# Optimization experiments

Measured on AMD Instinct MI355X. Metric: run time of the kernel, lower is better.

The kernel has to match this reference:

```python
import jax, jax.numpy as jnp
import numpy as np

V = 50000

def _spmm(edge_vals, edge_row, edge_col, x):
    # sparse (V,V) @ dense (V,F) via gather + segment_sum
    return jax.ops.segment_sum(edge_vals[:, None] * x[edge_col], edge_row, num_segments=V)

def setup_inputs() -> dict:
    key = jax.random.key(0)
    ks = jax.random.split(key, 6)
    B, Cin, Cout, K, E = 4, 128, 128, 4, 800000
    x = jax.random.normal(ks[0], (B, Cin, V), dtype=jnp.float32)
    edge_row = jax.random.randint(ks[1], (E,), 0, V, dtype=jnp.int32)
    edge_col = jax.random.randint(ks[2], (E,), 0, V, dtype=jnp.int32)
    edge_vals = jax.random.normal(ks[3], (E,), dtype=jnp.float32) * 0.05
    std = np.sqrt(2.0 / (Cin * K)).astype(np.float32)
    weights = jax.random.normal(ks[4], (K, Cin, Cout), dtype=jnp.float32) * std
    biases = jnp.full((Cout,), 0.01, dtype=jnp.float32)
    return {"x": x, "edge_row": edge_row, "edge_col": edge_col,
            "edge_vals": edge_vals, "weights": weights, "biases": biases}

def reference(x, edge_row, edge_col, edge_vals, weights, biases):
    B, Cin, Vv = x.shape
    K = weights.shape[0]
    # (B,Cin,V) -> (V, B*Cin)
    x0 = jnp.transpose(x, (2, 0, 1)).reshape(Vv, B * Cin)
    xs = [x0]
    if K > 1:
        x1 = _spmm(edge_vals, edge_row, edge_col, x0)
        xs.append(x1)
        for _ in range(2, K):
            x2 = 2.0 * _spmm(edge_vals, edge_row, edge_col, x1) - x0
            xs.append(x2)
            x0, x1 = x1, x2
    xk = jnp.stack(xs, 0).reshape(K, Vv, B, Cin)
    # tensordot over (K, Cin): (K,V,B,Cin) x (K,Cin,Cout) -> (V,B,Cout)
    out = jnp.einsum('kvbc,kco->vbo', xk, weights)
    out = out + biases
    # permute (V,B,Cout) -> (B,Cout,V)
    return jnp.transpose(out, (1, 2, 0))
```

## Files before the change

kernel.cpp:

```cpp
#include <hip/hip_runtime.h>

#define V_N   50000
#define B_N   4
#define C_IN  128
#define C_OUT 128
#define E_N   800000
#define F_N   512
#define M_TOT 200000

#define SCAN_BLK  1024
#define SCAN_NB   ((V_N + SCAN_BLK - 1) / SCAN_BLK)

typedef unsigned short ushort_t;
typedef __attribute__((ext_vector_type(8))) short short8;
typedef __attribute__((ext_vector_type(4))) float f32x4;

__device__ __forceinline__ float bf_lo(unsigned u) { return __uint_as_float(u << 16); }
__device__ __forceinline__ float bf_hi(unsigned u) { return __uint_as_float(u & 0xFFFF0000u); }
__device__ __forceinline__ ushort_t f2bf(float f) {
    unsigned u = __float_as_uint(f);
    u += 0x7FFFu + ((u >> 16) & 1u);
    return (ushort_t)(u >> 16);
}

__global__ __launch_bounds__(256) void k_transpose_in(const float* __restrict__ x,
                                                      ushort_t* __restrict__ x0) {
    __shared__ float tile[32][33];
    int vb = blockIdx.x * 32;
    int fb = blockIdx.y * 32;
    int tx = threadIdx.x, ty = threadIdx.y;
#pragma unroll
    for (int i = 0; i < 32; i += 8) {
        int f = fb + ty + i, v = vb + tx;
        float val = 0.f;
        if (v < V_N) val = x[(size_t)f * V_N + v];
        tile[ty + i][tx] = val;
    }
    __syncthreads();
#pragma unroll
    for (int i = 0; i < 32; i += 8) {
        int v = vb + ty + i, f = fb + tx;
        if (v < V_N) x0[(size_t)v * F_N + f] = f2bf(tile[tx][ty + i]);
    }
}

__global__ __launch_bounds__(256) void k_hist(const int* __restrict__ row,
                                              int* __restrict__ counts) {
    int e = blockIdx.x * blockDim.x + threadIdx.x;
    if (e < E_N) atomicAdd(&counts[row[e]], 1);
}

__global__ __launch_bounds__(256) void k_scan_blk(const int* __restrict__ counts,
                                                  int* __restrict__ row_ptr,
                                                  int* __restrict__ blk_sums) {
    __shared__ int s[256];
    int t = threadIdx.x;
    int base = blockIdx.x * SCAN_BLK + t * 4;
    int c0 = (base + 0 < V_N) ? counts[base + 0] : 0;
    int c1 = (base + 1 < V_N) ? counts[base + 1] : 0;
    int c2 = (base + 2 < V_N) ? counts[base + 2] : 0;
    int c3 = (base + 3 < V_N) ? counts[base + 3] : 0;
    int p1 = c0, p2 = c0 + c1, p3 = c0 + c1 + c2, tot = p3 + c3;
    s[t] = tot;
    __syncthreads();
#pragma unroll
    for (int off = 1; off < 256; off <<= 1) {
        int v = (t >= off) ? s[t - off] : 0;
        __syncthreads();
        s[t] += v;
        __syncthreads();
    }
    int excl = (t == 0) ? 0 : s[t - 1];
    if (base + 0 < V_N) row_ptr[base + 0] = excl;
    if (base + 1 < V_N) row_ptr[base + 1] = excl + p1;
    if (base + 2 < V_N) row_ptr[base + 2] = excl + p2;
    if (base + 3 < V_N) row_ptr[base + 3] = excl + p3;
    if (t == 255) blk_sums[blockIdx.x] = s[255];
}

__global__ __launch_bounds__(64) void k_scan_top(const int* __restrict__ blk_sums,
                                                 int* __restrict__ blk_off) {
    int t = threadIdx.x;
    int v = (t < SCAN_NB) ? blk_sums[t] : 0;
#pragma unroll
    for (int off = 1; off < 64; off <<= 1) {
        int u = __shfl_up(v, off);
        if (t >= off) v += u;
    }
    blk_off[t] = v;
}

__global__ __launch_bounds__(256) void k_scan_add(const int* __restrict__ blk_off,
                                                  int* __restrict__ row_ptr,
                                                  int* __restrict__ next) {
    int b = blockIdx.x, t = threadIdx.x;
    int off = (b == 0) ? 0 : blk_off[b - 1];
    int base = b * SCAN_BLK + t * 4;
#pragma unroll
    for (int i = 0; i < 4; i++) {
        int idx = base + i;
        if (idx < V_N) {
            int rv = row_ptr[idx] + off;
            row_ptr[idx] = rv;
            next[idx]    = rv;
        }
    }
    if (b == 0 && t == 0) row_ptr[V_N] = blk_off[SCAN_NB - 1];
}

__global__ __launch_bounds__(256) void k_scatter(const int* __restrict__ row,
                                                 const int* __restrict__ col,
                                                 const float* __restrict__ vals,
                                                 int* __restrict__ next,
                                                 int2* __restrict__ edges) {
    int e = blockIdx.x * blockDim.x + threadIdx.x;
    if (e < E_N) {
        int r = row[e];
        int pos = atomicAdd(&next[r], 1);
        edges[pos] = make_int2(col[e], __float_as_int(vals[e]));
    }
}

__global__ __launch_bounds__(256) void k_wprep(const float* __restrict__ W,
                                               ushort_t* __restrict__ Wt) {
    int i = blockIdx.x * 256 + threadIdx.x;
    int k = i >> 14, c = (i >> 7) & 127, o = i & 127;
    Wt[((size_t)k * 128 + o) * 128 + c] = f2bf(W[i]);
}

__global__ __launch_bounds__(256) void k_spmm_bf16(const int* __restrict__ row_ptr,
                                                   const int2* __restrict__ edges,
                                                   const ushort_t* __restrict__ src,
                                                   const ushort_t* __restrict__ prev,
                                                   ushort_t* __restrict__ dst,
                                                   float alpha, float beta,
                                                   int has_prev) {
    int lane = threadIdx.x & 63;
    int g = blockIdx.x * 4 + (threadIdx.x >> 6);
    int r = g >> 1;
    int h = g & 1;
    int e0 = row_ptr[r], e1 = row_ptr[r + 1];
    float a0 = 0.f, a1 = 0.f, a2 = 0.f, a3 = 0.f;
    const ushort_t* sp = src + h * 256 + lane * 4;

    int e = e0;
    for (; e + 4 <= e1; e += 4) {
        int2 E0 = edges[e], E1 = edges[e + 1], E2 = edges[e + 2], E3 = edges[e + 3];
        uint2 g0 = *(const uint2*)(sp + (size_t)E0.x * F_N);
        uint2 g1 = *(const uint2*)(sp + (size_t)E1.x * F_N);
        uint2 g2 = *(const uint2*)(sp + (size_t)E2.x * F_N);
        uint2 g3 = *(const uint2*)(sp + (size_t)E3.x * F_N);
        float w0 = __int_as_float(E0.y), w1 = __int_as_float(E1.y);
        float w2 = __int_as_float(E2.y), w3 = __int_as_float(E3.y);
        a0 += w0 * bf_lo(g0.x); a1 += w0 * bf_hi(g0.x);
        a2 += w0 * bf_lo(g0.y); a3 += w0 * bf_hi(g0.y);
        a0 += w1 * bf_lo(g1.x); a1 += w1 * bf_hi(g1.x);
        a2 += w1 * bf_lo(g1.y); a3 += w1 * bf_hi(g1.y);
        a0 += w2 * bf_lo(g2.x); a1 += w2 * bf_hi(g2.x);
        a2 += w2 * bf_lo(g2.y); a3 += w2 * bf_hi(g2.y);
        a0 += w3 * bf_lo(g3.x); a1 += w3 * bf_hi(g3.x);
        a2 += w3 * bf_lo(g3.y); a3 += w3 * bf_hi(g3.y);
    }
    for (; e < e1; e++) {
        int2 E = edges[e];
        uint2 gv = *(const uint2*)(sp + (size_t)E.x * F_N);
        float w = __int_as_float(E.y);
        a0 += w * bf_lo(gv.x); a1 += w * bf_hi(gv.x);
        a2 += w * bf_lo(gv.y); a3 += w * bf_hi(gv.y);
    }

    size_t off = (size_t)r * F_N + h * 256 + lane * 4;
    if (has_prev) {
        uint2 pv = *(const uint2*)(prev + off);
        a0 = alpha * a0 + beta * bf_lo(pv.x);
        a1 = alpha * a1 + beta * bf_hi(pv.x);
        a2 = alpha * a2 + beta * bf_lo(pv.y);
        a3 = alpha * a3 + beta * bf_hi(pv.y);
    } else {
        a0 *= alpha; a1 *= alpha; a2 *= alpha; a3 *= alpha;
    }
    ushort_t res[4] = {f2bf(a0), f2bf(a1), f2bf(a2), f2bf(a3)};
    *(uint2*)(dst + off) = *(const uint2*)res;
}

__global__ __launch_bounds__(256, 2) void k_gemm_mfma(
        const ushort_t* __restrict__ X0, const ushort_t* __restrict__ X1,
        const ushort_t* __restrict__ X2, const ushort_t* __restrict__ X3,
        const ushort_t* __restrict__ Wt, const float* __restrict__ bias,
        float* __restrict__ out) {
    __shared__ ushort_t As[128][40];
    __shared__ ushort_t Bs[128][40];
    __shared__ float    Cs[64][133];

    int tid  = threadIdx.x;
    int lane = tid & 63;
    int wave = tid >> 6;
    int wm = wave >> 1, wn = wave & 1;
    int quad = lane >> 4, l15 = lane & 15;
    int m_blk = blockIdx.x * 128;

    f32x4 acc[4][4];
#pragma unroll
    for (int fi = 0; fi < 4; fi++)
#pragma unroll
        for (int fj = 0; fj < 4; fj++) {
            acc[fi][fj][0] = 0.f; acc[fi][fj][1] = 0.f;
            acc[fi][fj][2] = 0.f; acc[fi][fj][3] = 0.f;
        }

    const ushort_t* Xb[4] = {X0, X1, X2, X3};

    for (int kb = 0; kb < 4; kb++) {
        const ushort_t* A = Xb[kb];
        const ushort_t* W = Wt + (size_t)kb * (128 * 128);
        for (int kk = 0; kk < 128; kk += 32) {
            __syncthreads();
#pragma unroll
            for (int i = 0; i < 2; i++) {
                int id = tid + i * 256;
                int rr = id >> 2, p = id & 3;
                int gm = m_blk + rr; if (gm >= M_TOT) gm = M_TOT - 1;
                *(uint4*)&As[rr][p * 8] = *(const uint4*)&A[(size_t)gm * 128 + kk + p * 8];
                *(uint4*)&Bs[rr][p * 8] = *(const uint4*)&W[(size_t)rr * 128 + kk + p * 8];
            }
            __syncthreads();
            short8 a[4], b[4];
#pragma unroll
            for (int f = 0; f < 4; f++) {
                a[f] = *(const short8*)&As[wm * 64 + f * 16 + l15][quad * 8];
                b[f] = *(const short8*)&Bs[wn * 64 + f * 16 + l15][quad * 8];
            }
#pragma unroll
            for (int fi = 0; fi < 4; fi++)
#pragma unroll
                for (int fj = 0; fj < 4; fj++)
                    acc[fi][fj] = __builtin_amdgcn_mfma_f32_16x16x32_bf16(
                        a[fi], b[fj], acc[fi][fj], 0, 0, 0);
        }
    }

    int v_blk = m_blk >> 2;
    for (int h = 0; h < 2; h++) {
        __syncthreads();
        if (wm == h) {
#pragma unroll
            for (int fi = 0; fi < 4; fi++)
#pragma unroll
                for (int fj = 0; fj < 4; fj++) {
                    int ml = fi * 16 + quad * 4;
                    int n  = wn * 64 + fj * 16 + l15;
#pragma unroll
                    for (int reg = 0; reg < 4; reg++)
                        Cs[ml + reg][n] = acc[fi][fj][reg];
                }
        }
        __syncthreads();
#pragma unroll
        for (int i = 0; i < 8; i++) {
            int idx = tid + i * 256;
            int v4  = idx & 3;
            int o   = (idx >> 2) & 127;
            int b   = idx >> 9;
            int vl  = v4 * 4;
            float bv = bias[o];
            float r0 = Cs[(vl + 0) * 4 + b][o] + bv;
            float r1 = Cs[(vl + 1) * 4 + b][o] + bv;
            float r2 = Cs[(vl + 2) * 4 + b][o] + bv;
            float r3 = Cs[(vl + 3) * 4 + b][o] + bv;
            int v0 = v_blk + h * 16 + vl;
            float* op = out + ((size_t)b * C_OUT + o) * V_N + v0;
            if (v0 + 3 < V_N) {
                *(float4*)op = make_float4(r0, r1, r2, r3);
            } else {
                if (v0     < V_N) op[0] = r0;
                if (v0 + 1 < V_N) op[1] = r1;
                if (v0 + 2 < V_N) op[2] = r2;
                if (v0 + 3 < V_N) op[3] = r3;
            }
        }
    }
}

extern "C" void kernel_launch(void* const* d_in, const int* in_sizes, int n_in,
                              void* d_out, int out_size, void* d_ws, size_t ws_size,
                              hipStream_t stream) {
    const float* x        = (const float*)d_in[0];
    const int*   edge_row = (const int*)  d_in[1];
    const int*   edge_col = (const int*)  d_in[2];
    const float* edge_val = (const float*)d_in[3];
    const float* weights  = (const float*)d_in[4];
    const float* biases   = (const float*)d_in[5];
    float* out = (float*)d_out;

    const size_t XSZ = (size_t)V_N * F_N;
    ushort_t* x0 = (ushort_t*)d_ws;
    ushort_t* x1 = x0 + XSZ;
    ushort_t* x2 = x1 + XSZ;
    ushort_t* x3 = x2 + XSZ;
    ushort_t* Wt = x3 + XSZ;
    int* iw      = (int*)(Wt + 4 * 128 * 128);
    int* row_ptr = iw;
    int* counts  = iw + 50016;
    int* nxt     = iw + 100032;
    int* blk_sums= iw + 150048;
    int* blk_off = iw + 150112;
    int2* edges  = (int2*)(iw + 150176);

    dim3 tb(32, 8);
    dim3 tgrid((V_N + 31) / 32, F_N / 32);

    k_transpose_in<<<tgrid, tb, 0, stream>>>(x, x0);

    hipMemsetAsync(counts, 0, V_N * sizeof(int), stream);
    k_hist<<<(E_N + 255) / 256, 256, 0, stream>>>(edge_row, counts);
    k_scan_blk<<<SCAN_NB, 256, 0, stream>>>(counts, row_ptr, blk_sums);
    k_scan_top<<<1, 64, 0, stream>>>(blk_sums, blk_off);
    k_scan_add<<<SCAN_NB, 256, 0, stream>>>(blk_off, row_ptr, nxt);
    k_scatter<<<(E_N + 255) / 256, 256, 0, stream>>>(edge_row, edge_col, edge_val,
                                                     nxt, edges);

    k_wprep<<<256, 256, 0, stream>>>(weights, Wt);

    k_spmm_bf16<<<V_N * 2 / 4, 256, 0, stream>>>(row_ptr, edges, x0, x0, x1,
                                                 1.f, 0.f, 0);
    k_spmm_bf16<<<V_N * 2 / 4, 256, 0, stream>>>(row_ptr, edges, x1, x0, x2,
                                                 2.f, -1.f, 1);
    k_spmm_bf16<<<V_N * 2 / 4, 256, 0, stream>>>(row_ptr, edges, x2, x1, x3,
                                                 2.f, -1.f, 1);

    k_gemm_mfma<<<(M_TOT + 127) / 128, 256, 0, stream>>>(x0, x1, x2, x3, Wt,
                                                         biases, out);
}
```

Before: 724.6 us.

## Use direct global-to-LDS loads with XOR swizzle and K=64 tiles in GEMM

The MFMA GEMM now loads A and W tiles straight into shared memory with global_load_lds (16-byte) instead of staging them through registers. K-steps are widened from 32 to 64, which halves the number of barrier pairs. An XOR swizzle on 16-byte column groups replaces the padded layout to avoid LDS bank conflicts. This adds LDS footprint (64-wide rows) and relies on the per-wave contiguous LDS write pattern of the direct-load instruction, but the GEMM is likely a minor part of a runtime dominated by the SpMM stages.

```diff
diff --git a/kernel.cpp b/kernel.cpp
--- a/kernel.cpp
+++ b/kernel.cpp
@@ -14,6 +14,13 @@
 typedef unsigned short ushort_t;
 typedef __attribute__((ext_vector_type(8))) short short8;
 typedef __attribute__((ext_vector_type(4))) float f32x4;
+
+#define AS1 __attribute__((address_space(1)))
+#define AS3 __attribute__((address_space(3)))
+__device__ __forceinline__ void gl_lds16(const void* gp, void* lp) {
+    __builtin_amdgcn_global_load_lds((const AS1 unsigned int*)gp,
+                                     (AS3 unsigned int*)lp, 16, 0, 0);
+}
 
 __device__ __forceinline__ float bf_lo(unsigned u) { return __uint_as_float(u << 16); }
 __device__ __forceinline__ float bf_hi(unsigned u) { return __uint_as_float(u & 0xFFFF0000u); }
@@ -188,14 +195,14 @@
         const ushort_t* __restrict__ X2, const ushort_t* __restrict__ X3,
         const ushort_t* __restrict__ Wt, const float* __restrict__ bias,
         float* __restrict__ out) {
-    __shared__ ushort_t As[128][40];
-    __shared__ ushort_t Bs[128][40];
+    __shared__ ushort_t As[128][64];
+    __shared__ ushort_t Bs[128][64];
     __shared__ float    Cs[64][133];
 
     int tid  = threadIdx.x;
     int lane = tid & 63;
-    int wave = tid >> 6;
-    int wm = wave >> 1, wn = wave & 1;
+    int wv   = tid >> 6;
+    int wm = wv >> 1, wn = wv & 1;
     int quad = lane >> 4, l15 = lane & 15;
     int m_blk = blockIdx.x * 128;
 
@@ -210,32 +217,44 @@
 
     const ushort_t* Xb[4] = {X0, X1, X2, X3};
 
+    int rr_s = lane >> 3;
+    int pl   = lane & 7;
     for (int kb = 0; kb < 4; kb++) {
         const ushort_t* A = Xb[kb];
         const ushort_t* W = Wt + (size_t)kb * (128 * 128);
-        for (int kk = 0; kk < 128; kk += 32) {
+        for (int kk = 0; kk < 128; kk += 64) {
             __syncthreads();
 #pragma unroll
-            for (int i = 0; i < 2; i++) {
-                int id = tid + i * 256;
-                int rr = id >> 2, p = id & 3;
+            for (int i = 0; i < 4; i++) {
+                int r0 = (wv * 4 + i) * 8;
+                int rr = r0 + rr_s;
+                int pg = pl ^ (rr & 7);
                 int gm = m_blk + rr; if (gm >= M_TOT) gm = M_TOT - 1;
-                *(uint4*)&As[rr][p * 8] = *(const uint4*)&A[(size_t)gm * 128 + kk + p * 8];
-                *(uint4*)&Bs[rr][p * 8] = *(const uint4*)&W[(size_t)rr * 128 + kk + p * 8];
+                gl_lds16(&A[(size_t)gm * 128 + kk + pg * 8], &As[r0][0]);
+                gl_lds16(&W[(size_t)rr * 128 + kk + pg * 8], &Bs[r0][0]);
             }
             __syncthreads();
-            short8 a[4], b[4];
-#pragma unroll
-            for (int f = 0; f < 4; f++) {
-                a[f] = *(const short8*)&As[wm * 64 + f * 16 + l15][quad * 8];
-                b[f] = *(const short8*)&Bs[wn * 64 + f * 16 + l15][quad * 8];
-            }
-#pragma unroll
-            for (int fi = 0; fi < 4; fi++)
-#pragma unroll
-                for (int fj = 0; fj < 4; fj++)
-                    acc[fi][fj] = __builtin_amdgcn_mfma_f32_16x16x32_bf16(
-                        a[fi], b[fj], acc[fi][fj], 0, 0, 0);
+
+            short8 a[2][4], b[2][4];
+#pragma unroll
+            for (int h = 0; h < 2; h++)
+#pragma unroll
+                for (int f = 0; f < 4; f++) {
+                    int ra = wm * 64 + f * 16 + l15;
+                    int ca = (h * 4 + quad) ^ (ra & 7);
+                    a[h][f] = *(const short8*)&As[ra][ca * 8];
+                    int rb = wn * 64 + f * 16 + l15;
+                    int cb = (h * 4 + quad) ^ (rb & 7);
+                    b[h][f] = *(const short8*)&Bs[rb][cb * 8];
+                }
+#pragma unroll
+            for (int h = 0; h < 2; h++)
+#pragma unroll
+                for (int fi = 0; fi < 4; fi++)
+#pragma unroll
+                    for (int fj = 0; fj < 4; fj++)
+                        acc[fi][fj] = __builtin_amdgcn_mfma_f32_16x16x32_bf16(
+                            a[h][fi], b[h][fj], acc[fi][fj], 0, 0, 0);
         }
     }
 
```

Result: faster. 698.9 us (-3.6%).
